# Kernel tuning notes

Hardware: AMD Instinct MI355X
Metric: run time of the kernel (lower is better)

The kernel has to match this reference:

```python
import jax, jax.numpy as jnp
import numpy as np


def setup_inputs() -> dict:
    key = jax.random.key(0)
    ks = jax.random.split(key, 13)
    B, W, C = 16, 2048, 512
    inp = {
        "X_sfr": jax.random.normal(ks[0], (B, W, C), dtype=jnp.float32),
        "adj_matrix": jax.random.normal(ks[1], (B, C, C), dtype=jnp.float32),
        "log_temp": jnp.zeros((1,), dtype=jnp.float32),
        "wq": jax.random.normal(ks[2], (1,), dtype=jnp.float32),
        "bq": jax.random.normal(ks[3], (1,), dtype=jnp.float32),
        "wk": jax.random.normal(ks[4], (1,), dtype=jnp.float32),
        "bk": jax.random.normal(ks[5], (1,), dtype=jnp.float32),
        "wv": jax.random.normal(ks[6], (1,), dtype=jnp.float32),
        "bv": jax.random.normal(ks[7], (1,), dtype=jnp.float32),
        "wmu": jax.random.normal(ks[8], (1,), dtype=jnp.float32),
        "bmu": jax.random.normal(ks[9], (1,), dtype=jnp.float32),
        "wsig": jax.random.normal(ks[10], (1,), dtype=jnp.float32),
        "bsig": jax.random.normal(ks[11], (1,), dtype=jnp.float32),
        "k1": 20,
        "k2": 30,
    }
    return inp


def reference(X_sfr, adj_matrix, log_temp, wq, bq, wk, bk, wv, bv, wmu, bmu, wsig, bsig, k1, k2):
    B, W, C = X_sfr.shape
    # spatial propagation: relu + in-degree normalize adjacency
    adj_nonneg = jnp.maximum(adj_matrix, 0.0)
    in_deg = jnp.clip(adj_nonneg.sum(axis=1, keepdims=True), 1e-4)  # [B,1,C]
    adj_norm = adj_nonneg / in_deg
    X_spatial = jnp.einsum('bwi,bij->bwj', X_sfr, adj_norm)  # [B,W,C]

    # static band mask over time: k1 <= |dt| <= k2, fallback to identity rows
    t = jnp.arange(W)
    delta = jnp.abs(t[None, :] - t[:, None])
    band = (delta >= k1) & (delta <= k2)  # [W,W]
    has_valid = band.any(axis=1)
    band = jnp.where(has_valid[:, None], band, jnp.eye(W, dtype=bool))

    # scalar (1->1) q/k/v projections on the temporal token
    temporal_token = X_spatial.mean(axis=2, keepdims=True)  # [B,W,1]
    q = wq * temporal_token + bq                            # [B,W,1]
    k = wk * temporal_token + bk                            # [B,W,1]
    v = wv * X_spatial + bv                                 # [B,W,C]

    temp = jax.nn.softplus(log_temp)[0] + 1e-4
    logits = jnp.matmul(q, jnp.swapaxes(k, 1, 2)) / temp    # [B,W,W] rank-1
    logits = jnp.where(band[None, :, :], logits, -1e9)
    attn = jax.nn.softmax(logits, axis=-1)
    attn = attn * band[None, :, :].astype(attn.dtype)
    attn = attn / (attn.sum(axis=-1, keepdims=True) + 1e-6)

    sacon_scalar = attn.sum(axis=-1, keepdims=True)         # [B,W,1]
    sacon = jnp.broadcast_to(sacon_scalar, (B, W, C))

    X_temporal = jnp.matmul(attn, v)                        # [B,W,C]
    X_fused = X_temporal + X_spatial

    mu = jnp.clip(wmu * X_fused + bmu, -20.0, 20.0)
    sigma_sq = jax.nn.softplus(wsig * X_fused + bsig) + 0.1
    return mu, sigma_sq, sacon
```

## Files before the change

### kernel.cpp

```cpp
#include <hip/hip_runtime.h>
#include <math.h>

#define B_ 16
#define W_ 2048
#define C_ 512

#define OFF_XB    0
#define OFF_BT    33554432
#define OFF_XSP   41943040
#define OFF_INDEG 75497472
#define OFF_TT    75530240

typedef short v8s __attribute__((ext_vector_type(8)));
typedef float v4f __attribute__((ext_vector_type(4)));

__device__ __forceinline__ float softplusf(float x) {
    return fmaxf(x, 0.f) + log1pf(expf(-fabsf(x)));
}
__device__ __forceinline__ unsigned short f2bf(float x) {
    unsigned int u = __float_as_uint(x);
    unsigned int r = (u + 0x7FFFu + ((u >> 16) & 1u)) >> 16;
    return (unsigned short)r;
}
__device__ __forceinline__ float bf2f(unsigned int h) {
    return __uint_as_float(h << 16);
}

__global__ void indeg_kernel(const float* __restrict__ adj, float* __restrict__ indeg) {
    int b = blockIdx.x;
    int j = blockIdx.y * 256 + threadIdx.x;
    int i0 = blockIdx.z * 64;
    const float* base = adj + (size_t)b * C_ * C_ + (size_t)i0 * C_ + j;
    float s = 0.f;
#pragma unroll 8
    for (int i = 0; i < 64; i++) s += fmaxf(base[(size_t)i * C_], 0.f);
    atomicAdd(&indeg[b * C_ + j], s);
}

__global__ void convertA(const float* __restrict__ X, ushort* __restrict__ Xb) {
    int idx = blockIdx.x * 256 + threadIdx.x;
    float4 v = ((const float4*)X)[idx];
    ushort4 o;
    o.x = f2bf(v.x); o.y = f2bf(v.y); o.z = f2bf(v.z); o.w = f2bf(v.w);
    ((ushort4*)Xb)[idx] = o;
}

__global__ void convertB(const float* __restrict__ adj, const float* __restrict__ indeg,
                         ushort* __restrict__ Bt) {
    __shared__ float t[32][33];
    int b = blockIdx.z, i0 = blockIdx.x * 32, j0 = blockIdx.y * 32;
    int tx = threadIdx.x & 31;
    int ty = threadIdx.x >> 5;
    const float* src = adj + (size_t)b * C_ * C_;
#pragma unroll
    for (int rr = 0; rr < 4; rr++) {
        int ii = ty + rr * 8;
        t[ii][tx] = fmaxf(src[(size_t)(i0 + ii) * C_ + j0 + tx], 0.f);
    }
    __syncthreads();
    int jr0 = threadIdx.x >> 4;
    int ic  = (threadIdx.x & 15) * 2;
#pragma unroll
    for (int pp = 0; pp < 2; pp++) {
        int jr = jr0 + pp * 16;
        float inv = 1.f / fmaxf(indeg[b * C_ + j0 + jr], 1e-4f);
        ushort2 o;
        o.x = f2bf(t[ic][jr] * inv);
        o.y = f2bf(t[ic + 1][jr] * inv);
        *(ushort2*)&Bt[(size_t)b * C_ * C_ + (size_t)(j0 + jr) * C_ + i0 + ic] = o;
    }
}

#define LDA 56
__global__ __launch_bounds__(256) void gemm_mfma(const ushort* __restrict__ Xb,
                                                 const ushort* __restrict__ Bt,
                                                 ushort* __restrict__ Xsp) {
    __shared__ ushort As[128 * LDA];
    __shared__ ushort Bs[128 * LDA];
    const int b  = blockIdx.z;
    const int m0 = blockIdx.y * 128;
    const int n0 = blockIdx.x * 128;
    const int tid  = threadIdx.x;
    const int wave = tid >> 6, lane = tid & 63;
    const int quad = lane >> 4, l16 = lane & 15;
    const int mw = (wave & 1) * 64, nw = (wave >> 1) * 64;

    const ushort* Ag = Xb + (size_t)b * W_ * C_ + (size_t)m0 * C_;
    const ushort* Bg = Bt + (size_t)b * C_ * C_ + (size_t)n0 * C_;

    const int sm = tid >> 2;
    const int sk = (tid & 3) * 8;

    v4f acc[4][4];
#pragma unroll
    for (int mt = 0; mt < 4; mt++)
#pragma unroll
        for (int nt = 0; nt < 4; nt++)
            acc[mt][nt] = (v4f){0.f, 0.f, 0.f, 0.f};

    for (int k0 = 0; k0 < C_; k0 += 32) {
        uint4 a0 = *(const uint4*)(Ag + (size_t)sm * C_ + k0 + sk);
        uint4 a1 = *(const uint4*)(Ag + (size_t)(sm + 64) * C_ + k0 + sk);
        uint4 b0 = *(const uint4*)(Bg + (size_t)sm * C_ + k0 + sk);
        uint4 b1 = *(const uint4*)(Bg + (size_t)(sm + 64) * C_ + k0 + sk);
        __syncthreads();
        *(uint4*)&As[sm * LDA + sk]        = a0;
        *(uint4*)&As[(sm + 64) * LDA + sk] = a1;
        *(uint4*)&Bs[sm * LDA + sk]        = b0;
        *(uint4*)&Bs[(sm + 64) * LDA + sk] = b1;
        __syncthreads();

        v8s af[4], bf[4];
#pragma unroll
        for (int mt = 0; mt < 4; mt++)
            af[mt] = *(const v8s*)&As[(mw + mt * 16 + l16) * LDA + quad * 8];
#pragma unroll
        for (int nt = 0; nt < 4; nt++)
            bf[nt] = *(const v8s*)&Bs[(nw + nt * 16 + l16) * LDA + quad * 8];
#pragma unroll
        for (int mt = 0; mt < 4; mt++)
#pragma unroll
            for (int nt = 0; nt < 4; nt++)
                acc[mt][nt] = __builtin_amdgcn_mfma_f32_16x16x32_bf16(af[mt], bf[nt], acc[mt][nt], 0, 0, 0);
    }

#pragma unroll
    for (int mt = 0; mt < 4; mt++) {
#pragma unroll
        for (int nt = 0; nt < 4; nt++) {
            int col = n0 + nw + nt * 16 + l16;
#pragma unroll
            for (int r = 0; r < 4; r++) {
                int row = m0 + mw + mt * 16 + quad * 4 + r;
                Xsp[((size_t)b * W_ + row) * C_ + col] = f2bf(acc[mt][nt][r]);
            }
        }
    }
}

__global__ void tt_kernel(const ushort* __restrict__ Xsp, float* __restrict__ tt) {
    int row  = blockIdx.x * 4 + (threadIdx.x >> 6);
    int lane = threadIdx.x & 63;
    uint4 v = *(const uint4*)(Xsp + (size_t)row * C_ + lane * 8);
    float s = bf2f(v.x & 0xffff) + bf2f(v.x >> 16)
            + bf2f(v.y & 0xffff) + bf2f(v.y >> 16)
            + bf2f(v.z & 0xffff) + bf2f(v.z >> 16)
            + bf2f(v.w & 0xffff) + bf2f(v.w >> 16);
#pragma unroll
    for (int off = 32; off > 0; off >>= 1) s += __shfl_xor(s, off);
    if (lane == 0) tt[row] = s * (1.f / C_);
}

__global__ __launch_bounds__(256) void final_kernel(const ushort* __restrict__ Xsp,
                                                    const float* __restrict__ tt,
                                                    const float* __restrict__ ltp,
                                                    const float* __restrict__ wqp, const float* __restrict__ bqp,
                                                    const float* __restrict__ wkp, const float* __restrict__ bkp,
                                                    const float* __restrict__ wvp, const float* __restrict__ bvp,
                                                    const float* __restrict__ wmup, const float* __restrict__ bmup,
                                                    const float* __restrict__ wsigp, const float* __restrict__ bsigp,
                                                    const int* __restrict__ k1p, const int* __restrict__ k2p,
                                                    float* __restrict__ out) {
    __shared__ float wlds[32];
    __shared__ float Slds;
    const int row = blockIdx.x;
    const int b = row >> 11, i = row & (W_ - 1);
    const int K1 = k1p[0], K2 = k2p[0];
    int ns = K2 - K1 + 1;
    if (ns > 16) ns = 16;
    const int n2 = 2 * ns;
    const int tid = threadIdx.x;

    if (tid < 32) {
        const float temp = softplusf(ltp[0]) + 1e-4f;
        const float invt = 1.f / temp;
        const float q = wqp[0] * tt[row] + bqp[0];
        const float wk = wkp[0], bk = bkp[0];
        const float* ttb = tt + b * W_;
        int s = tid;
        int j = (s < ns) ? (i - K2 + s) : (i + K1 + (s - ns));
        bool valid = (s < n2) && (j >= 0) && (j < W_);
        float l = valid ? (q * (wk * ttb[j] + bk) * invt) : -INFINITY;
        float mx = l;
#pragma unroll
        for (int off = 16; off > 0; off >>= 1) mx = fmaxf(mx, __shfl_xor(mx, off, 32));
        float e = valid ? expf(l - mx) : 0.f;
        float T = e;
#pragma unroll
        for (int off = 16; off > 0; off >>= 1) T += __shfl_xor(T, off, 32);
        float p = e / T;
        float S = p;
#pragma unroll
        for (int off = 16; off > 0; off >>= 1) S += __shfl_xor(S, off, 32);
        float rn = 1.f / (S + 1e-6f);
        wlds[tid] = p * rn;
        if (tid == 0) Slds = S * rn;
    }
    __syncthreads();

    const ushort* Xbp = Xsp + (size_t)b * W_ * C_;
    const int c2 = tid * 2;
    float a0 = 0.f, a1 = 0.f;
    for (int s = 0; s < n2; s++) {
        float w = wlds[s];
        int j = (s < ns) ? (i - K2 + s) : (i + K1 + (s - ns));
        j = min(max(j, 0), W_ - 1);
        unsigned int v = *(const unsigned int*)(Xbp + (size_t)j * C_ + c2);
        a0 = fmaf(w, bf2f(v & 0xffff), a0);
        a1 = fmaf(w, bf2f(v >> 16), a1);
    }
    const float S = Slds;
    const float wv = wvp[0], bv = bvp[0];
    const float wmu = wmup[0], bmu = bmup[0];
    const float wsig = wsigp[0], bsig = bsigp[0];

    unsigned int xv = *(const unsigned int*)(Xbp + (size_t)i * C_ + c2);
    const float xsp0 = bf2f(xv & 0xffff);
    const float xsp1 = bf2f(xv >> 16);
    const float xf0 = fmaf(wv, a0, bv * S) + xsp0;
    const float xf1 = fmaf(wv, a1, bv * S) + xsp1;

    float2 muv, sgv, scv;
    muv.x = fminf(fmaxf(fmaf(wmu, xf0, bmu), -20.f), 20.f);
    muv.y = fminf(fmaxf(fmaf(wmu, xf1, bmu), -20.f), 20.f);
    sgv.x = softplusf(fmaf(wsig, xf0, bsig)) + 0.1f;
    sgv.y = softplusf(fmaf(wsig, xf1, bsig)) + 0.1f;
    scv.x = S; scv.y = S;

    const size_t N = (size_t)B_ * W_ * C_;
    const size_t base = (size_t)row * C_ + c2;
    *(float2*)&out[base]         = muv;
    *(float2*)&out[N + base]     = sgv;
    *(float2*)&out[2 * N + base] = scv;
}

extern "C" void kernel_launch(void* const* d_in, const int* in_sizes, int n_in,
                              void* d_out, int out_size, void* d_ws, size_t ws_size,
                              hipStream_t stream) {
    const float* X_sfr = (const float*)d_in[0];
    const float* adj   = (const float*)d_in[1];
    const float* ltp   = (const float*)d_in[2];
    const float* wq    = (const float*)d_in[3];
    const float* bq    = (const float*)d_in[4];
    const float* wk    = (const float*)d_in[5];
    const float* bk    = (const float*)d_in[6];
    const float* wv    = (const float*)d_in[7];
    const float* bv    = (const float*)d_in[8];
    const float* wmu   = (const float*)d_in[9];
    const float* bmu   = (const float*)d_in[10];
    const float* wsig  = (const float*)d_in[11];
    const float* bsig  = (const float*)d_in[12];
    const int*   k1p   = (const int*)d_in[13];
    const int*   k2p   = (const int*)d_in[14];

    char* ws = (char*)d_ws;
    ushort* Xb    = (ushort*)(ws + OFF_XB);
    ushort* Bt    = (ushort*)(ws + OFF_BT);
    ushort* Xsp   = (ushort*)(ws + OFF_XSP);
    float*  indeg = (float*)(ws + OFF_INDEG);
    float*  tt    = (float*)(ws + OFF_TT);
    float*  out   = (float*)d_out;

    hipMemsetAsync(indeg, 0, B_ * C_ * sizeof(float), stream);

    indeg_kernel<<<dim3(B_, C_ / 256, 8), 256, 0, stream>>>(adj, indeg);

    convertA<<<(B_ * W_ * C_ / 4) / 256, 256, 0, stream>>>(X_sfr, Xb);

    convertB<<<dim3(C_ / 32, C_ / 32, B_), 256, 0, stream>>>(adj, indeg, Bt);

    gemm_mfma<<<dim3(C_ / 128, W_ / 128, B_), 256, 0, stream>>>(Xb, Bt, Xsp);

    tt_kernel<<<(B_ * W_) / 4, 256, 0, stream>>>(Xsp, tt);

    final_kernel<<<B_ * W_, 256, 0, stream>>>(Xsp, tt, ltp, wq, bq, wk, bk,
                                              wv, bv, wmu, bmu, wsig, bsig,
                                              k1p, k2p, out);
}
```

Baseline: 419.2 us.

## Fuse row-mean into GEMM epilogue, use direct global-to-LDS loads, widen final kernel

The GEMM now stages tiles through global_load_lds directly into unpadded LDS instead of going through registers. Its epilogue also reduces each output row's partial sums with shuffles and atomically adds them into the temporal-token buffer, which removes the separate tt_kernel pass over Xsp. The final kernel now handles four rows per block with one wave per row, using 16-byte loads and stores instead of 4/8-byte ones. Risks: the unpadded LDS layout may cause bank conflicts on the MFMA fragment reads, the atomics add contention, and the fp32 sums come from accumulators before bf16 rounding, so values differ slightly.

Measured after the change: 391.1 us. 6.7% less time.

```diff
diff --git a/kernel.cpp b/kernel.cpp
--- a/kernel.cpp
+++ b/kernel.cpp
@@ -13,6 +13,7 @@
 
 typedef short v8s __attribute__((ext_vector_type(8)));
 typedef float v4f __attribute__((ext_vector_type(4)));
+typedef unsigned int u32;
 
 __device__ __forceinline__ float softplusf(float x) {
     return fmaxf(x, 0.f) + log1pf(expf(-fabsf(x)));
@@ -24,6 +25,11 @@
 }
 __device__ __forceinline__ float bf2f(unsigned int h) {
     return __uint_as_float(h << 16);
+}
+__device__ __forceinline__ void gload16(const ushort* g, ushort* l) {
+    __builtin_amdgcn_global_load_lds(
+        (const __attribute__((address_space(1))) u32*)(g),
+        (__attribute__((address_space(3))) u32*)(l), 16, 0, 0);
 }
 
 __global__ void indeg_kernel(const float* __restrict__ adj, float* __restrict__ indeg) {
@@ -71,12 +77,12 @@
     }
 }
 
-#define LDA 56
 __global__ __launch_bounds__(256) void gemm_mfma(const ushort* __restrict__ Xb,
                                                  const ushort* __restrict__ Bt,
-                                                 ushort* __restrict__ Xsp) {
-    __shared__ ushort As[128 * LDA];
-    __shared__ ushort Bs[128 * LDA];
+                                                 ushort* __restrict__ Xsp,
+                                                 float* __restrict__ tt) {
+    __shared__ ushort As[128 * 32];
+    __shared__ ushort Bs[128 * 32];
     const int b  = blockIdx.z;
     const int m0 = blockIdx.y * 128;
     const int n0 = blockIdx.x * 128;
@@ -99,24 +105,20 @@
             acc[mt][nt] = (v4f){0.f, 0.f, 0.f, 0.f};
 
     for (int k0 = 0; k0 < C_; k0 += 32) {
-        uint4 a0 = *(const uint4*)(Ag + (size_t)sm * C_ + k0 + sk);
-        uint4 a1 = *(const uint4*)(Ag + (size_t)(sm + 64) * C_ + k0 + sk);
-        uint4 b0 = *(const uint4*)(Bg + (size_t)sm * C_ + k0 + sk);
-        uint4 b1 = *(const uint4*)(Bg + (size_t)(sm + 64) * C_ + k0 + sk);
         __syncthreads();
-        *(uint4*)&As[sm * LDA + sk]        = a0;
-        *(uint4*)&As[(sm + 64) * LDA + sk] = a1;
-        *(uint4*)&Bs[sm * LDA + sk]        = b0;
-        *(uint4*)&Bs[(sm + 64) * LDA + sk] = b1;
+        gload16(Ag + (size_t)sm * C_ + k0 + sk,        As + tid * 8);
+        gload16(Ag + (size_t)(sm + 64) * C_ + k0 + sk, As + 2048 + tid * 8);
+        gload16(Bg + (size_t)sm * C_ + k0 + sk,        Bs + tid * 8);
+        gload16(Bg + (size_t)(sm + 64) * C_ + k0 + sk, Bs + 2048 + tid * 8);
         __syncthreads();
 
         v8s af[4], bf[4];
 #pragma unroll
         for (int mt = 0; mt < 4; mt++)
-            af[mt] = *(const v8s*)&As[(mw + mt * 16 + l16) * LDA + quad * 8];
+            af[mt] = *(const v8s*)&As[(mw + mt * 16 + l16) * 32 + quad * 8];
 #pragma unroll
         for (int nt = 0; nt < 4; nt++)
-            bf[nt] = *(const v8s*)&Bs[(nw + nt * 16 + l16) * LDA + quad * 8];
+            bf[nt] = *(const v8s*)&Bs[(nw + nt * 16 + l16) * 32 + quad * 8];
 #pragma unroll
         for (int mt = 0; mt < 4; mt++)
 #pragma unroll
@@ -136,19 +138,22 @@
             }
         }
     }
-}
-
-__global__ void tt_kernel(const ushort* __restrict__ Xsp, float* __restrict__ tt) {
-    int row  = blockIdx.x * 4 + (threadIdx.x >> 6);
-    int lane = threadIdx.x & 63;
-    uint4 v = *(const uint4*)(Xsp + (size_t)row * C_ + lane * 8);
-    float s = bf2f(v.x & 0xffff) + bf2f(v.x >> 16)
-            + bf2f(v.y & 0xffff) + bf2f(v.y >> 16)
-            + bf2f(v.z & 0xffff) + bf2f(v.z >> 16)
-            + bf2f(v.w & 0xffff) + bf2f(v.w >> 16);
-#pragma unroll
-    for (int off = 32; off > 0; off >>= 1) s += __shfl_xor(s, off);
-    if (lane == 0) tt[row] = s * (1.f / C_);
+
+#pragma unroll
+    for (int mt = 0; mt < 4; mt++) {
+#pragma unroll
+        for (int r = 0; r < 4; r++) {
+            float s = acc[mt][0][r] + acc[mt][1][r] + acc[mt][2][r] + acc[mt][3][r];
+            s += __shfl_xor(s, 1);
+            s += __shfl_xor(s, 2);
+            s += __shfl_xor(s, 4);
+            s += __shfl_xor(s, 8);
+            if (l16 == 0) {
+                int row = m0 + mw + mt * 16 + quad * 4 + r;
+                atomicAdd(&tt[b * W_ + row], s);
+            }
+        }
+    }
 }
 
 __global__ __launch_bounds__(256) void final_kernel(const ushort* __restrict__ Xsp,
@@ -161,23 +166,24 @@
                                                     const float* __restrict__ wsigp, const float* __restrict__ bsigp,
                                                     const int* __restrict__ k1p, const int* __restrict__ k2p,
                                                     float* __restrict__ out) {
-    __shared__ float wlds[32];
-    __shared__ float Slds;
-    const int row = blockIdx.x;
+    __shared__ float wsh[4][32];
+    __shared__ float Ssh[4];
+    const int wid = threadIdx.x >> 6, lane = threadIdx.x & 63;
+    const int row = blockIdx.x * 4 + wid;
     const int b = row >> 11, i = row & (W_ - 1);
     const int K1 = k1p[0], K2 = k2p[0];
     int ns = K2 - K1 + 1;
     if (ns > 16) ns = 16;
     const int n2 = 2 * ns;
-    const int tid = threadIdx.x;
-
-    if (tid < 32) {
+
+    if (lane < 32) {
+        const float cinv = 1.f / C_;
         const float temp = softplusf(ltp[0]) + 1e-4f;
         const float invt = 1.f / temp;
-        const float q = wqp[0] * tt[row] + bqp[0];
-        const float wk = wkp[0], bk = bkp[0];
+        const float q = (wqp[0] * cinv) * tt[row] + bqp[0];
+        const float wk = wkp[0] * cinv, bk = bkp[0];
         const float* ttb = tt + b * W_;
-        int s = tid;
+        int s = lane;
         int j = (s < ns) ? (i - K2 + s) : (i + K1 + (s - ns));
         bool valid = (s < n2) && (j >= 0) && (j < W_);
         float l = valid ? (q * (wk * ttb[j] + bk) * invt) : -INFINITY;
@@ -193,45 +199,56 @@
 #pragma unroll
         for (int off = 16; off > 0; off >>= 1) S += __shfl_xor(S, off, 32);
         float rn = 1.f / (S + 1e-6f);
-        wlds[tid] = p * rn;
-        if (tid == 0) Slds = S * rn;
+        wsh[wid][lane] = p * rn;
+        if (lane == 0) Ssh[wid] = S * rn;
     }
     __syncthreads();
 
     const ushort* Xbp = Xsp + (size_t)b * W_ * C_;
-    const int c2 = tid * 2;
-    float a0 = 0.f, a1 = 0.f;
+    const int c8 = lane * 8;
+    float a[8] = {0.f, 0.f, 0.f, 0.f, 0.f, 0.f, 0.f, 0.f};
     for (int s = 0; s < n2; s++) {
-        float w = wlds[s];
+        float w = wsh[wid][s];
         int j = (s < ns) ? (i - K2 + s) : (i + K1 + (s - ns));
         j = min(max(j, 0), W_ - 1);
-        unsigned int v = *(const unsigned int*)(Xbp + (size_t)j * C_ + c2);
-        a0 = fmaf(w, bf2f(v & 0xffff), a0);
-        a1 = fmaf(w, bf2f(v >> 16), a1);
-    }
-    const float S = Slds;
+        uint4 v = *(const uint4*)(Xbp + (size_t)j * C_ + c8);
+        a[0] = fmaf(w, bf2f(v.x & 0xffff), a[0]);
+        a[1] = fmaf(w, bf2f(v.x >> 16),    a[1]);
+        a[2] = fmaf(w, bf2f(v.y & 0xffff), a[2]);
+        a[3] = fmaf(w, bf2f(v.y >> 16),    a[3]);
+        a[4] = fmaf(w, bf2f(v.z & 0xffff), a[4]);
+        a[5] = fmaf(w, bf2f(v.z >> 16),    a[5]);
+        a[6] = fmaf(w, bf2f(v.w & 0xffff), a[6]);
+        a[7] = fmaf(w, bf2f(v.w >> 16),    a[7]);
+    }
+    const float S = Ssh[wid];
     const float wv = wvp[0], bv = bvp[0];
     const float wmu = wmup[0], bmu = bmup[0];
     const float wsig = wsigp[0], bsig = bsigp[0];
 
-    unsigned int xv = *(const unsigned int*)(Xbp + (size_t)i * C_ + c2);
-    const float xsp0 = bf2f(xv & 0xffff);
-    const float xsp1 = bf2f(xv >> 16);
-    const float xf0 = fmaf(wv, a0, bv * S) + xsp0;
-    const float xf1 = fmaf(wv, a1, bv * S) + xsp1;
-
-    float2 muv, sgv, scv;
-    muv.x = fminf(fmaxf(fmaf(wmu, xf0, bmu), -20.f), 20.f);
-    muv.y = fminf(fmaxf(fmaf(wmu, xf1, bmu), -20.f), 20.f);
-    sgv.x = softplusf(fmaf(wsig, xf0, bsig)) + 0.1f;
-    sgv.y = softplusf(fmaf(wsig, xf1, bsig)) + 0.1f;
-    scv.x = S; scv.y = S;
+    uint4 xv = *(const uint4*)(Xbp + (size_t)i * C_ + c8);
+    float xs[8];
+    xs[0] = bf2f(xv.x & 0xffff); xs[1] = bf2f(xv.x >> 16);
+    xs[2] = bf2f(xv.y & 0xffff); xs[3] = bf2f(xv.y >> 16);
+    xs[4] = bf2f(xv.z & 0xffff); xs[5] = bf2f(xv.z >> 16);
+    xs[6] = bf2f(xv.w & 0xffff); xs[7] = bf2f(xv.w >> 16);
+
+    float mu[8], sg[8];
+#pragma unroll
+    for (int k = 0; k < 8; k++) {
+        float xf = fmaf(wv, a[k], bv * S) + xs[k];
+        mu[k] = fminf(fmaxf(fmaf(wmu, xf, bmu), -20.f), 20.f);
+        sg[k] = softplusf(fmaf(wsig, xf, bsig)) + 0.1f;
+    }
 
     const size_t N = (size_t)B_ * W_ * C_;
-    const size_t base = (size_t)row * C_ + c2;
-    *(float2*)&out[base]         = muv;
-    *(float2*)&out[N + base]     = sgv;
-    *(float2*)&out[2 * N + base] = scv;
+    const size_t base = (size_t)row * C_ + c8;
+    *(float4*)&out[base]     = (float4){mu[0], mu[1], mu[2], mu[3]};
+    *(float4*)&out[base + 4] = (float4){mu[4], mu[5], mu[6], mu[7]};
+    *(float4*)&out[N + base]     = (float4){sg[0], sg[1], sg[2], sg[3]};
+    *(float4*)&out[N + base + 4] = (float4){sg[4], sg[5], sg[6], sg[7]};
+    *(float4*)&out[2 * N + base]     = (float4){S, S, S, S};
+    *(float4*)&out[2 * N + base + 4] = (float4){S, S, S, S};
 }
 
 extern "C" void kernel_launch(void* const* d_in, const int* in_sizes, int n_in,
@@ -261,7 +278,7 @@
     float*  tt    = (float*)(ws + OFF_TT);
     float*  out   = (float*)d_out;
 
-    hipMemsetAsync(indeg, 0, B_ * C_ * sizeof(float), stream);
+    hipMemsetAsync(indeg, 0, (B_ * C_ + B_ * W_) * sizeof(float), stream);
 
     indeg_kernel<<<dim3(B_, C_ / 256, 8), 256, 0, stream>>>(adj, indeg);
 
@@ -269,11 +286,9 @@
 
     convertB<<<dim3(C_ / 32, C_ / 32, B_), 256, 0, stream>>>(adj, indeg, Bt);
 
-    gemm_mfma<<<dim3(C_ / 128, W_ / 128, B_), 256, 0, stream>>>(Xb, Bt, Xsp);
-
-    tt_kernel<<<(B_ * W_) / 4, 256, 0, stream>>>(Xsp, tt);
-
-    final_kernel<<<B_ * W_, 256, 0, stream>>>(Xsp, tt, ltp, wq, bq, wk, bk,
-                                              wv, bv, wmu, bmu, wsig, bsig,
-                                              k1p, k2p, out);
-}
+    gemm_mfma<<<dim3(C_ / 128, W_ / 128, B_), 256, 0, stream>>>(Xb, Bt, Xsp, tt);
+
+    final_kernel<<<(B_ * W_) / 4, 256, 0, stream>>>(Xsp, tt, ltp, wq, bq, wk, bk,
+                                                    wv, bv, wmu, bmu, wsig, bsig,
+                                                    k1p, k2p, out);
+}
```
